# Kernel tuning notes

Measured on AMD Instinct MI355X. Metric: run time of the kernel, lower is better.

## Reference

```python
import jax, jax.numpy as jnp
import numpy as np

N, E, M, A, D = 100000, 3200000, 4096, 32, 16
G, V1, V2, O1 = 10, 20, 10, 20


def _lin(key, fin, fout, scale=0.1):
    kw, kb = jax.random.split(key)
    W = jax.random.normal(kw, (fin, fout), jnp.float32) * scale
    b = jax.random.normal(kb, (fout,), jnp.float32) * scale
    return W, b


def setup_inputs():
    key = jax.random.key(0)
    ks = jax.random.split(key, 32)
    inp = {}
    inp["x1"] = jax.random.normal(ks[0], (N, 15), jnp.float32)
    inp["x2"] = jax.random.normal(ks[1], (4,), jnp.float32)
    inp["edges"] = jax.random.randint(ks[2], (2, E), 0, N)
    inp["attack_src"] = jax.random.randint(ks[3], (M, A), 0, N)
    inp["attack_dst"] = jax.random.randint(ks[4], (M, A), 0, N)
    inp["attack_armies"] = jax.random.uniform(ks[5], (M, A), jnp.float32, 1.0, 20.0)
    inp["deploy_target"] = jax.random.randint(ks[6], (M, D), 0, N)
    inp["deploy_armies"] = jax.random.uniform(ks[7], (M, D), jnp.float32, 1.0, 10.0)
    inp["init_W"], inp["init_b"] = _lin(ks[8], 15, G)
    for i, fin in zip((1, 2, 3), (G + 15, 2 * G + 15, 3 * G + 15)):
        k1, k2, k3, k4 = jax.random.split(ks[8 + i], 4)
        inp[f"g{i}_Wl"] = jax.random.normal(k1, (fin, G), jnp.float32) * 0.1
        inp[f"g{i}_Wr"] = jax.random.normal(k2, (fin, G), jnp.float32) * 0.1
        inp[f"g{i}_att"] = jax.random.normal(k3, (G,), jnp.float32) * 0.1
        inp[f"g{i}_b"] = jax.random.normal(k4, (G,), jnp.float32) * 0.1
    inp["vt_W"], inp["vt_b"] = _lin(ks[12], 15 + G + 4, V1)
    inp["va_W"], inp["va_b"] = _lin(ks[13], V1, 1)
    inp["vv_W"], inp["vv_b"] = _lin(ks[14], V1, V2)
    inp["vl_W"], inp["vl_b"] = _lin(ks[15], V2, 1)
    inp["at_W"], inp["at_b"] = _lin(ks[16], 48, O1)
    inp["dt_W"], inp["dt_b"] = _lin(ks[17], 23, O1)
    inp["oa_W"], inp["oa_b"] = _lin(ks[18], O1, 1)
    inp["ov_W"], inp["ov_b"] = _lin(ks[19], O1, 1)
    return inp


def _gatv2(x, src, dst, Wl, Wr, att, bias, n):
    # GATv2 (PyG defaults: heads=1, negative_slope=0.2); dropout omitted (eval mode)
    xl = x @ Wl  # source-side transform  [N, G]
    xr = x @ Wr  # target-side transform  [N, G]
    e = jax.nn.leaky_relu(xl[src] + xr[dst], 0.2) @ att  # [Etot]
    emax = jax.ops.segment_max(e, dst, num_segments=n)
    ex = jnp.exp(e - emax[dst])
    denom = jax.ops.segment_sum(ex, dst, num_segments=n)
    alpha = ex / denom[dst]  # edge softmax per target node
    return jax.ops.segment_sum(alpha[:, None] * xl[src], dst, num_segments=n) + bias


def _forward(x1, x2, edges, attack_src, attack_dst, attack_armies,
             deploy_target, deploy_armies, p):
    n = x1.shape[0]
    loop = jnp.arange(n)
    src = jnp.concatenate([edges[0], loop])  # add_self_loops (PyG default)
    dst = jnp.concatenate([edges[1], loop])
    x_ = jax.nn.relu(x1 @ p["init_W"] + p["init_b"])  # Dropout = identity in eval
    xa = jax.nn.relu(_gatv2(jnp.concatenate([x_, x1], 1), src, dst,
                            p["g1_Wl"], p["g1_Wr"], p["g1_att"], p["g1_b"], n))
    xb = jax.nn.relu(_gatv2(jnp.concatenate([xa, x_, x1], 1), src, dst,
                            p["g2_Wl"], p["g2_Wr"], p["g2_att"], p["g2_b"], n))
    xc = jax.nn.relu(_gatv2(jnp.concatenate([xb, xa, x_, x1], 1), src, dst,
                            p["g3_Wl"], p["g3_Wr"], p["g3_att"], p["g3_b"], n))
    # per-move order features, batched over all moves at once: [M,A,*] / [M,D,*]
    x1d = x1[attack_dst]  # [M, A, 15]
    extra = 0.6 * attack_armies - 0.7 * (x1d[..., 3] + x1d[..., 4])
    att_feat = jnp.concatenate([xc[attack_src], xc[attack_dst],
                                x1[attack_src][..., 3:], x1d[..., 1:],
                                attack_armies[..., None], extra[..., None]], -1)  # [M,A,48]
    dep_feat = jnp.concatenate([xc[deploy_target], x1[deploy_target][..., 3:],
                                deploy_armies[..., None]], -1)  # [M,D,23]
    orders = jax.nn.relu(jnp.concatenate(
        [att_feat @ p["at_W"] + p["at_b"], dep_feat @ p["dt_W"] + p["dt_b"]], 1))  # [M,A+D,O1]
    oattn = jax.nn.softmax(orders @ p["oa_W"] + p["oa_b"], axis=1)  # softmax over orders
    pm = jnp.sum(oattn * (orders @ p["ov_W"] + p["ov_b"]), axis=(1, 2))  # [M]
    # value head: attention-pool over nodes
    vfeat = jnp.concatenate([xc, x1, jnp.tile(x2, (n, 1))], 1)  # [N, 29]
    v = jax.nn.relu(vfeat @ p["vt_W"] + p["vt_b"])
    vattn = jax.nn.softmax(v @ p["va_W"] + p["va_b"], axis=0)
    vagg = jax.nn.relu(jnp.sum(vattn * (v @ p["vv_W"] + p["vv_b"]), axis=0))
    V = jnp.tanh(vagg @ p["vl_W"] + p["vl_b"]).reshape(())
    return V, jax.nn.log_softmax(pm)


def reference(x1, x2, edges, attack_src, attack_dst, attack_armies,
              deploy_target, deploy_armies,
              init_W, init_b,
              g1_Wl, g1_Wr, g1_att, g1_b,
              g2_Wl, g2_Wr, g2_att, g2_b,
              g3_Wl, g3_Wr, g3_att, g3_b,
              vt_W, vt_b, va_W, va_b, vv_W, vv_b, vl_W, vl_b,
              at_W, at_b, dt_W, dt_b, oa_W, oa_b, ov_W, ov_b):
    p = dict(init_W=init_W, init_b=init_b,
             g1_Wl=g1_Wl, g1_Wr=g1_Wr, g1_att=g1_att, g1_b=g1_b,
             g2_Wl=g2_Wl, g2_Wr=g2_Wr, g2_att=g2_att, g2_b=g2_b,
             g3_Wl=g3_Wl, g3_Wr=g3_Wr, g3_att=g3_att, g3_b=g3_b,
             vt_W=vt_W, vt_b=vt_b, va_W=va_W, va_b=va_b, vv_W=vv_W, vv_b=vv_b,
             vl_W=vl_W, vl_b=vl_b, at_W=at_W, at_b=at_b, dt_W=dt_W, dt_b=dt_b,
             oa_W=oa_W, oa_b=oa_b, ov_W=ov_W, ov_b=ov_b)
    return _forward(x1, x2, edges, attack_src, attack_dst, attack_armies,
                    deploy_target, deploy_armies, p)
```

## Files before the change

kernel.cpp:

```cpp
#include <hip/hip_runtime.h>
#include <math.h>


#define PAD 12
#define LP 8
#define MAXB 784
#define CHK 8192

__device__ __forceinline__ float lrelu02(float v) { return v > 0.f ? v : 0.2f * v; }

__device__ __forceinline__ unsigned pk_bf16(float a, float b)
{
    unsigned ua = __float_as_uint(a), ub = __float_as_uint(b);
    ua += 0x7fffu + ((ua >> 16) & 1u);
    ub += 0x7fffu + ((ub >> 16) & 1u);
    return (ua >> 16) | (ub & 0xffff0000u);
}
__device__ __forceinline__ float bf_lo(unsigned u) { return __uint_as_float(u << 16); }
__device__ __forceinline__ float bf_hi(unsigned u) { return __uint_as_float(u & 0xffff0000u); }

template <int NS>
__device__ __forceinline__ void transform_body(
    int n, const float* __restrict__ s0, const float* __restrict__ s1,
    const float* __restrict__ s2, const float* __restrict__ x1,
    const float* __restrict__ Wl, const float* __restrict__ Wr,
    unsigned* __restrict__ XLb, float* __restrict__ XR)
{
    float al[10], ar[10];
#pragma unroll
    for (int g = 0; g < 10; ++g) { al[g] = 0.f; ar[g] = 0.f; }
    int o = 0;
#define TB_BLOCK(SP)                                                        \
    {                                                                       \
        const float4* pr = (const float4*)((SP) + n * PAD);                 \
        float4 v0 = pr[0], v1 = pr[1], v2 = pr[2];                          \
        float fv[10] = {v0.x, v0.y, v0.z, v0.w, v1.x, v1.y, v1.z, v1.w,     \
                        v2.x, v2.y};                                        \
        _Pragma("unroll") for (int k = 0; k < 10; ++k)                      \
        {                                                                   \
            _Pragma("unroll") for (int g = 0; g < 10; ++g)                  \
            {                                                               \
                al[g] += fv[k] * Wl[(o + k) * 10 + g];                      \
                ar[g] += fv[k] * Wr[(o + k) * 10 + g];                      \
            }                                                               \
        }                                                                   \
        o += 10;                                                            \
    }
    if constexpr (NS >= 1) TB_BLOCK(s0)
    if constexpr (NS >= 2) TB_BLOCK(s1)
    if constexpr (NS >= 3) TB_BLOCK(s2)
#undef TB_BLOCK
#pragma unroll
    for (int k = 0; k < 15; ++k) {
        float fv = x1[n * 15 + k];
#pragma unroll
        for (int g = 0; g < 10; ++g) {
            al[g] += fv * Wl[(o + k) * 10 + g];
            ar[g] += fv * Wr[(o + k) * 10 + g];
        }
    }
    uint4 q0;
    q0.x = pk_bf16(al[0], al[1]);
    q0.y = pk_bf16(al[2], al[3]);
    q0.z = pk_bf16(al[4], al[5]);
    q0.w = pk_bf16(al[6], al[7]);
    uint4 q1;
    q1.x = pk_bf16(al[8], al[9]);
    q1.y = 0; q1.z = 0; q1.w = 0;
    uint4* pb = (uint4*)(XLb + (size_t)n * LP);
    pb[0] = q0;
    pb[1] = q1;
    float4* po = (float4*)(XR + n * PAD);
    po[0] = make_float4(ar[0], ar[1], ar[2], ar[3]);
    po[1] = make_float4(ar[4], ar[5], ar[6], ar[7]);
    po[2] = make_float4(ar[8], ar[9], 0.f, 0.f);
}

__global__ __launch_bounds__(256) void k_a1_init(
    const int* __restrict__ edst, int E, unsigned short* __restrict__ pos,
    int* __restrict__ cntg, int PA,
    const float* __restrict__ x1, const float* __restrict__ W,
    const float* __restrict__ b, float* __restrict__ xo, int N, int NBK)
{
    if ((int)blockIdx.x < PA) {
        __shared__ int h[MAXB];
        for (int j = threadIdx.x; j < NBK; j += 256) h[j] = 0;
        __syncthreads();
        int base = blockIdx.x * CHK;
        for (int k = 0; k < CHK / 256; ++k) {
            int i = base + k * 256 + threadIdx.x;
            if (i < E) {
                int bkt = edst[i] >> 7;
                int p = atomicAdd(&h[bkt], 1);
                pos[i] = (unsigned short)p;
            }
        }
        __syncthreads();
        for (int j = threadIdx.x; j < NBK; j += 256)
            cntg[(size_t)j * PA + blockIdx.x] = h[j];
    } else {
        int n = ((int)blockIdx.x - PA) * 256 + (int)threadIdx.x;
        if (n >= N) return;
        float acc[10];
#pragma unroll
        for (int g = 0; g < 10; ++g) acc[g] = b[g];
#pragma unroll
        for (int k = 0; k < 15; ++k) {
            float fv = x1[n * 15 + k];
#pragma unroll
            for (int g = 0; g < 10; ++g) acc[g] += fv * W[k * 10 + g];
        }
        float4* po = (float4*)(xo + n * PAD);
        po[0] = make_float4(fmaxf(acc[0], 0.f), fmaxf(acc[1], 0.f),
                            fmaxf(acc[2], 0.f), fmaxf(acc[3], 0.f));
        po[1] = make_float4(fmaxf(acc[4], 0.f), fmaxf(acc[5], 0.f),
                            fmaxf(acc[6], 0.f), fmaxf(acc[7], 0.f));
        po[2] = make_float4(fmaxf(acc[8], 0.f), fmaxf(acc[9], 0.f), 0.f, 0.f);
    }
}

__global__ __launch_bounds__(1024) void k_scanA(
    const int* __restrict__ cntg, int* __restrict__ bases,
    int* __restrict__ bsumA, int TOT)
{
    __shared__ int wsum[16];
    int t = threadIdx.x;
    int i = blockIdx.x * 1024 + t;
    int lane = t & 63, w = t >> 6;
    int x = (i < TOT) ? cntg[i] : 0;
    int incl = x;
#pragma unroll
    for (int off = 1; off < 64; off <<= 1) {
        int u = __shfl_up(incl, off);
        if (lane >= off) incl += u;
    }
    if (lane == 63) wsum[w] = incl;
    __syncthreads();
    int woff = 0;
    for (int k = 0; k < w; ++k) woff += wsum[k];
    incl += woff;
    if (i < TOT) bases[i] = incl - x;
    if (t == 1023) bsumA[blockIdx.x] = incl;
}

__global__ __launch_bounds__(512) void k_scanB(
    const int* __restrict__ bsumA, int* __restrict__ boffA, int NBLKA,
    float* __restrict__ vsums, int* __restrict__ rowptr, int N, int Etot)
{
    __shared__ int wsum[8];
    int t = threadIdx.x;
    int lane = t & 63, w = t >> 6;
    int x = (t < NBLKA) ? bsumA[t] : 0;
    int incl = x;
#pragma unroll
    for (int off = 1; off < 64; off <<= 1) {
        int u = __shfl_up(incl, off);
        if (lane >= off) incl += u;
    }
    if (lane == 63) wsum[w] = incl;
    __syncthreads();
    int woff = 0;
    for (int k = 0; k < w; ++k) woff += wsum[k];
    incl += woff;
    if (t < NBLKA) boffA[t] = incl - x;
    if (t < 16) vsums[t] = 0.f;
    if (t == 0) rowptr[N] = Etot;
}

__global__ __launch_bounds__(1024) void k_scanC(
    int* __restrict__ bases, const int* __restrict__ boffA, int TOT)
{
    int i = blockIdx.x * 1024 + threadIdx.x;
    if (i < TOT) bases[i] += boffA[blockIdx.x];
}

__global__ __launch_bounds__(256) void k_a2(
    const int* __restrict__ esrc, const int* __restrict__ edst, int E,
    const int* __restrict__ bases, const unsigned short* __restrict__ pos,
    unsigned* __restrict__ pairs, int PA)
{
    int i = blockIdx.x * 256 + threadIdx.x;
    if (i >= E) return;
    int d = edst[i], s = esrc[i];
    int bkt = d >> 7;
    int blk = i / CHK;
    int dest = bases[(size_t)bkt * PA + blk] + (int)pos[i];
    pairs[dest] = (unsigned)s | ((unsigned)(d & 127) << 17);
}

__global__ __launch_bounds__(256) void k_b_tr1(
    const unsigned* __restrict__ pairs, const int* __restrict__ bases,
    int* __restrict__ rowptr, int* __restrict__ deg, int* __restrict__ sidx,
    int N, int NBK, int PA, int E,
    const float* __restrict__ s0a, const float* __restrict__ x1,
    const float* __restrict__ Wl, const float* __restrict__ Wr,
    unsigned* __restrict__ XLb, float* __restrict__ XR, int NB)
{
    if ((int)blockIdx.x < NBK) {
        __shared__ int cnt[128];
        __shared__ int cur[128];
        __shared__ int wtot;
        int t = threadIdx.x;
        if (t < 128) cnt[t] = 0;
        __syncthreads();
        int b = blockIdx.x;
        int p0 = bases[(size_t)b * PA];
        int p1 = (b + 1 < NBK) ? bases[(size_t)(b + 1) * PA] : E;
        int n0 = b << 7;
        int nn = N - n0; nn = nn < 0 ? 0 : (nn > 128 ? 128 : nn);
        for (int i = p0 + t; i < p1; i += 256) atomicAdd(&cnt[pairs[i] >> 17], 1);
        __syncthreads();
        int x = 0, incl = 0;
        if (t < 128) {
            x = cnt[t] + (t < nn ? 1 : 0);
            incl = x;
            int lane = t & 63;
#pragma unroll
            for (int off = 1; off < 64; off <<= 1) {
                int u = __shfl_up(incl, off);
                if (lane >= off) incl += u;
            }
            if (t == 63) wtot = incl;
        }
        __syncthreads();
        int sb = p0 + (b << 7);
        if (t < 128) {
            if (t >= 64) incl += wtot;
            int st = incl - x;
            if (t < nn) {
                int r = sb + st;
                rowptr[n0 + t] = r;
                deg[n0 + t] = cnt[t] + 1;
                sidx[r] = n0 + t;
                cur[t] = st + 1;
            } else {
                cur[t] = st;
            }
        }
        __syncthreads();
        for (int i = p0 + t; i < p1; i += 256) {
            unsigned w = pairs[i];
            int l = w >> 17, s = w & 0x1FFFF;
            int off = atomicAdd(&cur[l], 1);
            sidx[sb + off] = s;
        }
    } else {
        int n = ((int)blockIdx.x - NBK) * 256 + (int)threadIdx.x;
        if (n >= N) return;
        transform_body<1>(n, s0a, nullptr, nullptr, x1, Wl, Wr, XLb, XR);
    }
}

template <int NS>
__global__ __launch_bounds__(256) void k_transform(
    const float* __restrict__ s0, const float* __restrict__ s1,
    const float* __restrict__ s2, const float* __restrict__ x1,
    const float* __restrict__ Wl, const float* __restrict__ Wr,
    unsigned* __restrict__ XLb, float* __restrict__ XR, int N)
{
    int n = blockIdx.x * blockDim.x + threadIdx.x;
    if (n >= N) return;
    transform_body<NS>(n, s0, s1, s2, x1, Wl, Wr, XLb, XR);
}

__global__ __launch_bounds__(256) void k_gather(
    const int* __restrict__ rowptr, const int* __restrict__ deg,
    const int* __restrict__ sidx,
    const unsigned* __restrict__ XLb, const float* __restrict__ XR,
    const float* __restrict__ att, const float* __restrict__ b,
    float* __restrict__ xo, int N)
{
    int node = blockIdx.x * 16 + (threadIdx.x >> 4);
    int l16 = threadIdx.x & 15;
    float acc[10];
#pragma unroll
    for (int g = 0; g < 10; ++g) acc[g] = 0.f;
    float den = 0.f;
    float satt[10];
#pragma unroll
    for (int g = 0; g < 10; ++g) satt[g] = att[g];
    if (node < N) {
        const float4* pr = (const float4*)(XR + node * PAD);
        float4 r0 = pr[0], r1 = pr[1], r2 = pr[2];
        float xr[10] = {r0.x, r0.y, r0.z, r0.w, r1.x, r1.y, r1.z, r1.w, r2.x, r2.y};
        int start = rowptr[node];
        int dgr = deg[node];
        int j = l16;
        while (j + 16 < dgr) {
            int s0 = sidx[start + j];
            int s1 = sidx[start + j + 16];
            const unsigned* pl0 = XLb + (size_t)s0 * LP;
            const unsigned* pl1 = XLb + (size_t)s1 * LP;
            uint4 qa = *(const uint4*)pl0;
            unsigned qa4 = pl0[4];
            uint4 qb = *(const uint4*)pl1;
            unsigned qb4 = pl1[4];
            float xa[10] = {bf_lo(qa.x), bf_hi(qa.x), bf_lo(qa.y), bf_hi(qa.y),
                            bf_lo(qa.z), bf_hi(qa.z), bf_lo(qa.w), bf_hi(qa.w),
                            bf_lo(qa4), bf_hi(qa4)};
            float xb[10] = {bf_lo(qb.x), bf_hi(qb.x), bf_lo(qb.y), bf_hi(qb.y),
                            bf_lo(qb.z), bf_hi(qb.z), bf_lo(qb.w), bf_hi(qb.w),
                            bf_lo(qb4), bf_hi(qb4)};
            float ea = 0.f, eb = 0.f;
#pragma unroll
            for (int g = 0; g < 10; ++g) {
                ea += lrelu02(xa[g] + xr[g]) * satt[g];
                eb += lrelu02(xb[g] + xr[g]) * satt[g];
            }
            float exa = __expf(ea), exb = __expf(eb);
#pragma unroll
            for (int g = 0; g < 10; ++g) acc[g] += exa * xa[g] + exb * xb[g];
            den += exa + exb;
            j += 32;
        }
        if (j < dgr) {
            int s = sidx[start + j];
            const unsigned* pl = XLb + (size_t)s * LP;
            uint4 q = *(const uint4*)pl;
            unsigned q4 = pl[4];
            float xl[10] = {bf_lo(q.x), bf_hi(q.x), bf_lo(q.y), bf_hi(q.y),
                            bf_lo(q.z), bf_hi(q.z), bf_lo(q.w), bf_hi(q.w),
                            bf_lo(q4), bf_hi(q4)};
            float e = 0.f;
#pragma unroll
            for (int g = 0; g < 10; ++g) e += lrelu02(xl[g] + xr[g]) * satt[g];
            float ex = __expf(e);
#pragma unroll
            for (int g = 0; g < 10; ++g) acc[g] += ex * xl[g];
            den += ex;
        }
    }
#pragma unroll
    for (int off = 1; off < 16; off <<= 1) {
        den += __shfl_xor(den, off);
#pragma unroll
        for (int g = 0; g < 10; ++g) acc[g] += __shfl_xor(acc[g], off);
    }
    if (node < N && l16 == 0) {
        float inv = 1.f / den;
        float r[10];
#pragma unroll
        for (int g = 0; g < 10; ++g) r[g] = fmaxf(acc[g] * inv + b[g], 0.f);
        float4* po = (float4*)(xo + node * PAD);
        po[0] = make_float4(r[0], r[1], r[2], r[3]);
        po[1] = make_float4(r[4], r[5], r[6], r[7]);
        po[2] = make_float4(r[8], r[9], 0.f, 0.f);
    }
}

__global__ __launch_bounds__(256) void k_scores(
    const float* __restrict__ xc, const float* __restrict__ x1,
    const float* __restrict__ x2,
    const int* __restrict__ asrc, const int* __restrict__ adst,
    const float* __restrict__ aarm,
    const int* __restrict__ dtgt, const float* __restrict__ darm,
    const float* __restrict__ atW, const float* __restrict__ atb,
    const float* __restrict__ dtW, const float* __restrict__ dtb,
    const float* __restrict__ oaW, const float* __restrict__ oab,
    const float* __restrict__ ovW, const float* __restrict__ ovb,
    const float* __restrict__ vtW, const float* __restrict__ vtb,
    const float* __restrict__ vaW, const float* __restrict__ vab,
    const float* __restrict__ vvW, const float* __restrict__ vvb,
    float* __restrict__ vsums, float2* __restrict__ OS,
    int AB, int DB, int NB, int N, int M)
{
    if ((int)blockIdx.x < AB) {
        int i = blockIdx.x * 256 + threadIdx.x;
        if (i >= M * 32) return;
        int m = i >> 5, a = i & 31;
        int s = asrc[i], d = adst[i];
        float arm = aarm[i];
        float ord[20];
#pragma unroll
        for (int j = 0; j < 20; ++j) ord[j] = atb[j];
        {
            const float4* pc = (const float4*)(xc + s * PAD);
            float4 c0 = pc[0], c1 = pc[1], c2 = pc[2];
            float fv[10] = {c0.x, c0.y, c0.z, c0.w, c1.x, c1.y, c1.z, c1.w,
                            c2.x, c2.y};
#pragma unroll
            for (int k = 0; k < 10; ++k)
#pragma unroll
                for (int j = 0; j < 20; ++j) ord[j] += fv[k] * atW[k * 20 + j];
        }
        {
            const float4* pc = (const float4*)(xc + d * PAD);
            float4 c0 = pc[0], c1 = pc[1], c2 = pc[2];
            float fv[10] = {c0.x, c0.y, c0.z, c0.w, c1.x, c1.y, c1.z, c1.w,
                            c2.x, c2.y};
#pragma unroll
            for (int k = 0; k < 10; ++k)
#pragma unroll
                for (int j = 0; j < 20; ++j)
                    ord[j] += fv[k] * atW[(10 + k) * 20 + j];
        }
#pragma unroll
        for (int k = 0; k < 12; ++k) {
            float fv = x1[s * 15 + 3 + k];
#pragma unroll
            for (int j = 0; j < 20; ++j) ord[j] += fv * atW[(20 + k) * 20 + j];
        }
        float d3 = 0.f, d4 = 0.f;
#pragma unroll
        for (int k = 0; k < 14; ++k) {
            float fv = x1[d * 15 + 1 + k];
            if (k == 2) d3 = fv;
            if (k == 3) d4 = fv;
#pragma unroll
            for (int j = 0; j < 20; ++j) ord[j] += fv * atW[(32 + k) * 20 + j];
        }
        float extra = 0.6f * arm - 0.7f * (d3 + d4);
#pragma unroll
        for (int j = 0; j < 20; ++j)
            ord[j] += arm * atW[46 * 20 + j] + extra * atW[47 * 20 + j];
        float asc = oab[0], vsc = ovb[0];
#pragma unroll
        for (int j = 0; j < 20; ++j) {
            float oj = fmaxf(ord[j], 0.f);
            asc += oj * oaW[j];
            vsc += oj * ovW[j];
        }
        OS[(size_t)m * 48 + a] = make_float2(asc, vsc);
    } else if ((int)blockIdx.x < AB + DB) {
        int i = ((int)blockIdx.x - AB) * 256 + threadIdx.x;
        if (i >= M * 16) return;
        int m = i >> 4, dd = i & 15;
        int tg = dtgt[i];
        float arm = darm[i];
        float ord[20];
#pragma unroll
        for (int j = 0; j < 20; ++j) ord[j] = dtb[j];
        {
            const float4* pc = (const float4*)(xc + tg * PAD);
            float4 c0 = pc[0], c1 = pc[1], c2 = pc[2];
            float fv[10] = {c0.x, c0.y, c0.z, c0.w, c1.x, c1.y, c1.z, c1.w,
                            c2.x, c2.y};
#pragma unroll
            for (int k = 0; k < 10; ++k)
#pragma unroll
                for (int j = 0; j < 20; ++j) ord[j] += fv[k] * dtW[k * 20 + j];
        }
#pragma unroll
        for (int k = 0; k < 12; ++k) {
            float fv = x1[tg * 15 + 3 + k];
#pragma unroll
            for (int j = 0; j < 20; ++j) ord[j] += fv * dtW[(10 + k) * 20 + j];
        }
#pragma unroll
        for (int j = 0; j < 20; ++j) ord[j] += arm * dtW[22 * 20 + j];
        float asc = oab[0], vsc = ovb[0];
#pragma unroll
        for (int j = 0; j < 20; ++j) {
            float oj = fmaxf(ord[j], 0.f);
            asc += oj * oaW[j];
            vsc += oj * ovW[j];
        }
        OS[(size_t)m * 48 + 32 + dd] = make_float2(asc, vsc);
    } else {
        __shared__ float sred[4][11];
        int t = threadIdx.x;
        int n = ((int)blockIdx.x - AB - DB) * 256 + t;
        float w = 0.f;
        float wv[10];
#pragma unroll
        for (int c = 0; c < 10; ++c) wv[c] = 0.f;
        if (n < N) {
            float v[20];
#pragma unroll
            for (int j = 0; j < 20; ++j) v[j] = vtb[j];
            {
                const float4* pc = (const float4*)(xc + n * PAD);
                float4 c0 = pc[0], c1 = pc[1], c2 = pc[2];
                float fv[10] = {c0.x, c0.y, c0.z, c0.w, c1.x, c1.y, c1.z, c1.w,
                                c2.x, c2.y};
#pragma unroll
                for (int k = 0; k < 10; ++k)
#pragma unroll
                    for (int j = 0; j < 20; ++j) v[j] += fv[k] * vtW[k * 20 + j];
            }
#pragma unroll
            for (int k = 0; k < 15; ++k) {
                float fv = x1[n * 15 + k];
#pragma unroll
                for (int j = 0; j < 20; ++j) v[j] += fv * vtW[(10 + k) * 20 + j];
            }
#pragma unroll
            for (int k = 0; k < 4; ++k) {
                float fv = x2[k];
#pragma unroll
                for (int j = 0; j < 20; ++j) v[j] += fv * vtW[(25 + k) * 20 + j];
            }
            float sc = vab[0];
#pragma unroll
            for (int j = 0; j < 20; ++j) {
                v[j] = fmaxf(v[j], 0.f);
                sc += v[j] * vaW[j];
            }
            w = __expf(sc);
#pragma unroll
            for (int c = 0; c < 10; ++c) {
                float t2 = vvb[c];
#pragma unroll
                for (int j = 0; j < 20; ++j) t2 += v[j] * vvW[j * 10 + c];
                wv[c] = w * t2;
            }
        }
#pragma unroll
        for (int off = 32; off > 0; off >>= 1) {
            w += __shfl_xor(w, off);
#pragma unroll
            for (int c = 0; c < 10; ++c) wv[c] += __shfl_xor(wv[c], off);
        }
        int wave = t >> 6, lane = t & 63;
        if (lane == 0) {
            sred[wave][0] = w;
#pragma unroll
            for (int c = 0; c < 10; ++c) sred[wave][1 + c] = wv[c];
        }
        __syncthreads();
        if (t == 0) {
#pragma unroll
            for (int c = 0; c < 11; ++c) {
                float s = sred[0][c] + sred[1][c] + sred[2][c] + sred[3][c];
                atomicAdd(&vsums[c], s);
            }
        }
    }
}

__global__ __launch_bounds__(256) void k_moves(
    const float2* __restrict__ OS, float* __restrict__ pm, int M)
{
    int m = blockIdx.x * 256 + threadIdx.x;
    if (m >= M) return;
    const float2* p = OS + (size_t)m * 48;
    float mx = -1e30f;
#pragma unroll
    for (int o = 0; o < 48; ++o) mx = fmaxf(mx, p[o].x);
    float Z = 0.f, num = 0.f;
#pragma unroll
    for (int o = 0; o < 48; ++o) {
        float e = __expf(p[o].x - mx);
        Z += e;
        num += e * p[o].y;
    }
    pm[m] = num / Z;
}

__global__ __launch_bounds__(1024) void k_final(
    const float* __restrict__ pm, const float* __restrict__ vsums,
    const float* __restrict__ vlW, const float* __restrict__ vlb,
    float* __restrict__ out, int M)
{
    __shared__ float red[16];
    __shared__ float sval;
    int t = threadIdx.x;
    int wave = t >> 6, lane = t & 63;
    if (t == 1023) {
        float inv = 1.f / vsums[0];
        float V = vlb[0];
#pragma unroll
        for (int j = 0; j < 10; ++j) V += fmaxf(vsums[1 + j] * inv, 0.f) * vlW[j];
        out[0] = tanhf(V);
    }
    float mx = -1e30f;
    for (int i = t; i < M; i += 1024) mx = fmaxf(mx, pm[i]);
#pragma unroll
    for (int off = 32; off > 0; off >>= 1) mx = fmaxf(mx, __shfl_xor(mx, off));
    if (lane == 0) red[wave] = mx;
    __syncthreads();
    if (t == 0) {
        float m2 = red[0];
        for (int i = 1; i < 16; ++i) m2 = fmaxf(m2, red[i]);
        sval = m2;
    }
    __syncthreads();
    float smax = sval;
    float sum = 0.f;
    for (int i = t; i < M; i += 1024) sum += __expf(pm[i] - smax);
#pragma unroll
    for (int off = 32; off > 0; off >>= 1) sum += __shfl_xor(sum, off);
    if (lane == 0) red[wave] = sum;
    __syncthreads();
    if (t == 0) {
        float s2 = 0.f;
        for (int i = 0; i < 16; ++i) s2 += red[i];
        sval = s2;
    }
    __syncthreads();
    float lse = smax + logf(sval);
    for (int i = t; i < M; i += 1024) out[1 + i] = pm[i] - lse;
}

extern "C" void kernel_launch(void* const* d_in, const int* in_sizes, int n_in,
                              void* d_out, int out_size, void* d_ws, size_t ws_size,
                              hipStream_t stream)
{
    const float* x1   = (const float*)d_in[0];
    const float* x2   = (const float*)d_in[1];
    const int*   edges = (const int*)d_in[2];
    const int*   asrc = (const int*)d_in[3];
    const int*   adst = (const int*)d_in[4];
    const float* aarm = (const float*)d_in[5];
    const int*   dtgt = (const int*)d_in[6];
    const float* darm = (const float*)d_in[7];
    const float* initW = (const float*)d_in[8];
    const float* initb = (const float*)d_in[9];
    const float* g1Wl = (const float*)d_in[10];
    const float* g1Wr = (const float*)d_in[11];
    const float* g1att = (const float*)d_in[12];
    const float* g1b = (const float*)d_in[13];
    const float* g2Wl = (const float*)d_in[14];
    const float* g2Wr = (const float*)d_in[15];
    const float* g2att = (const float*)d_in[16];
    const float* g2b = (const float*)d_in[17];
    const float* g3Wl = (const float*)d_in[18];
    const float* g3Wr = (const float*)d_in[19];
    const float* g3att = (const float*)d_in[20];
    const float* g3b = (const float*)d_in[21];
    const float* vtW = (const float*)d_in[22];
    const float* vtb = (const float*)d_in[23];
    const float* vaW = (const float*)d_in[24];
    const float* vab = (const float*)d_in[25];
    const float* vvW = (const float*)d_in[26];
    const float* vvb = (const float*)d_in[27];
    const float* vlW = (const float*)d_in[28];
    const float* vlb = (const float*)d_in[29];
    const float* atW = (const float*)d_in[30];
    const float* atb = (const float*)d_in[31];
    const float* dtW = (const float*)d_in[32];
    const float* dtb = (const float*)d_in[33];
    const float* oaW = (const float*)d_in[34];
    const float* oab = (const float*)d_in[35];
    const float* ovW = (const float*)d_in[36];
    const float* ovb = (const float*)d_in[37];

    const int N = in_sizes[0] / 15;
    const int E = in_sizes[2] / 2;
    const int M = in_sizes[3] / 32;
    const int Etot = E + N;
    const int NBK = (N + 127) >> 7;
    const int PA = (E + CHK - 1) / CHK;
    const int TOT = NBK * PA;

    float* ws = (float*)d_ws;
    size_t off = 0;
    float* XU = ws + off; off += (size_t)N * PAD;
    float* XA = ws + off; off += (size_t)N * PAD;
    float* XB = ws + off; off += (size_t)N * PAD;
    float* XC = ws + off; off += (size_t)N * PAD;
    unsigned* XLb = (unsigned*)(ws + off); off += (size_t)N * LP;
    float* XR = ws + off; off += (size_t)N * PAD;
    int* sidx = (int*)(ws + off); off += Etot;
    unsigned* pairs = (unsigned*)(ws + off); off += E;
    int* deg = (int*)(ws + off); off += N;
    int* rowptr = (int*)(ws + off); off += N + 8;
    int* cntg = (int*)(ws + off); off += TOT + 8;
    int* bases = (int*)(ws + off); off += TOT + 8;
    int* bsumA = (int*)(ws + off); off += 512;
    int* boffA = (int*)(ws + off); off += 512;
    float* VS = ws + off; off += 16;
    float* PM = ws + off; off += M;
    float2* OS = (float2*)(ws + off); off += (size_t)M * 48 * 2;
    unsigned short* pos = (unsigned short*)XA;

    float* outp = (float*)d_out;

    const int NB = (N + 255) / 256;
    const int NG = (N + 15) / 16;
    const int AB = (M * 32 + 255) / 256;
    const int DB = (M * 16 + 255) / 256;
    const int SCA = (TOT + 1023) / 1024;
    const int* esrc = edges;
    const int* edst = edges + E;

    k_a1_init<<<PA + NB, 256, 0, stream>>>(edst, E, pos, cntg, PA,
                                           x1, initW, initb, XU, N, NBK);
    k_scanA<<<SCA, 1024, 0, stream>>>(cntg, bases, bsumA, TOT);
    k_scanB<<<1, 512, 0, stream>>>(bsumA, boffA, SCA, VS, rowptr, N, Etot);
    k_scanC<<<SCA, 1024, 0, stream>>>(bases, boffA, TOT);
    k_a2<<<(E + 255) / 256, 256, 0, stream>>>(esrc, edst, E, bases, pos, pairs, PA);
    k_b_tr1<<<NBK + NB, 256, 0, stream>>>(pairs, bases, rowptr, deg, sidx, N, NBK, PA, E,
                                          XU, x1, g1Wl, g1Wr, XLb, XR, NB);
    k_gather<<<NG, 256, 0, stream>>>(rowptr, deg, sidx, XLb, XR, g1att, g1b, XA, N);

    k_transform<2><<<NB, 256, 0, stream>>>(XA, XU, nullptr, x1, g2Wl, g2Wr, XLb, XR, N);
    k_gather<<<NG, 256, 0, stream>>>(rowptr, deg, sidx, XLb, XR, g2att, g2b, XB, N);

    k_transform<3><<<NB, 256, 0, stream>>>(XB, XA, XU, x1, g3Wl, g3Wr, XLb, XR, N);
    k_gather<<<NG, 256, 0, stream>>>(rowptr, deg, sidx, XLb, XR, g3att, g3b, XC, N);

    k_scores<<<AB + DB + NB, 256, 0, stream>>>(XC, x1, x2, asrc, adst, aarm,
                                               dtgt, darm, atW, atb, dtW, dtb,
                                               oaW, oab, ovW, ovb,
                                               vtW, vtb, vaW, vab, vvW, vvb,
                                               VS, OS, AB, DB, NB, N, M);
    k_moves<<<(M + 255) / 256, 256, 0, stream>>>(OS, PM, M);
    k_final<<<1, 1024, 0, stream>>>(PM, VS, vlW, vlb, outp, M);
}
```

Before: 405.2 us.

## Locally sort edge chunks in shared memory before scattering to bucket pairs

The scatter pass now re-histograms each edge chunk in LDS, scans the bucket counts locally, and sorts the chunk's edges by bucket in shared memory before writing them. Writes to the global pairs array therefore land in contiguous runs per bucket instead of random addresses, and the global pos array is no longer needed. The chunk size is halved so the larger per-block shared memory fits and there are more blocks, which doubles the number of partial histograms to scan. The first layer transform moves to run alongside this scatter pass instead of the CSR build, adding LDS use and an extra block-wide scan per chunk.

```diff
diff --git a/kernel.cpp b/kernel.cpp
--- a/kernel.cpp
+++ b/kernel.cpp
@@ -5,7 +5,7 @@
 #define PAD 12
 #define LP 8
 #define MAXB 784
-#define CHK 8192
+#define CHK 4096
 
 __device__ __forceinline__ float lrelu02(float v) { return v > 0.f ? v : 0.2f * v; }
 
@@ -77,8 +77,7 @@
 }
 
 __global__ __launch_bounds__(256) void k_a1_init(
-    const int* __restrict__ edst, int E, unsigned short* __restrict__ pos,
-    int* __restrict__ cntg, int PA,
+    const int* __restrict__ edst, int E, int* __restrict__ cntg, int PA,
     const float* __restrict__ x1, const float* __restrict__ W,
     const float* __restrict__ b, float* __restrict__ xo, int N, int NBK)
 {
@@ -89,11 +88,7 @@
         int base = blockIdx.x * CHK;
         for (int k = 0; k < CHK / 256; ++k) {
             int i = base + k * 256 + threadIdx.x;
-            if (i < E) {
-                int bkt = edst[i] >> 7;
-                int p = atomicAdd(&h[bkt], 1);
-                pos[i] = (unsigned short)p;
-            }
+            if (i < E) atomicAdd(&h[edst[i] >> 7], 1);
         }
         __syncthreads();
         for (int j = threadIdx.x; j < NBK; j += 256)
@@ -143,11 +138,11 @@
     if (t == 1023) bsumA[blockIdx.x] = incl;
 }
 
-__global__ __launch_bounds__(512) void k_scanB(
+__global__ __launch_bounds__(1024) void k_scanB(
     const int* __restrict__ bsumA, int* __restrict__ boffA, int NBLKA,
     float* __restrict__ vsums, int* __restrict__ rowptr, int N, int Etot)
 {
-    __shared__ int wsum[8];
+    __shared__ int wsum[16];
     int t = threadIdx.x;
     int lane = t & 63, w = t >> 6;
     int x = (t < NBLKA) ? bsumA[t] : 0;
@@ -174,80 +169,140 @@
     if (i < TOT) bases[i] += boffA[blockIdx.x];
 }
 
-__global__ __launch_bounds__(256) void k_a2(
+__global__ __launch_bounds__(256) void k_a2tr1(
     const int* __restrict__ esrc, const int* __restrict__ edst, int E,
-    const int* __restrict__ bases, const unsigned short* __restrict__ pos,
-    unsigned* __restrict__ pairs, int PA)
-{
-    int i = blockIdx.x * 256 + threadIdx.x;
-    if (i >= E) return;
-    int d = edst[i], s = esrc[i];
-    int bkt = d >> 7;
-    int blk = i / CHK;
-    int dest = bases[(size_t)bkt * PA + blk] + (int)pos[i];
-    pairs[dest] = (unsigned)s | ((unsigned)(d & 127) << 17);
-}
-
-__global__ __launch_bounds__(256) void k_b_tr1(
-    const unsigned* __restrict__ pairs, const int* __restrict__ bases,
-    int* __restrict__ rowptr, int* __restrict__ deg, int* __restrict__ sidx,
-    int N, int NBK, int PA, int E,
+    const int* __restrict__ bases, unsigned* __restrict__ pairs, int PA,
     const float* __restrict__ s0a, const float* __restrict__ x1,
     const float* __restrict__ Wl, const float* __restrict__ Wr,
-    unsigned* __restrict__ XLb, float* __restrict__ XR, int NB)
-{
-    if ((int)blockIdx.x < NBK) {
-        __shared__ int cnt[128];
-        __shared__ int cur[128];
-        __shared__ int wtot;
+    unsigned* __restrict__ XLb, float* __restrict__ XR, int N, int NBK)
+{
+    __shared__ int h[MAXB];
+    __shared__ unsigned tmp[CHK];
+    __shared__ unsigned vals[CHK];
+    __shared__ unsigned short bkt16[CHK];
+    __shared__ int wtotS[4];
+    if ((int)blockIdx.x < PA) {
         int t = threadIdx.x;
-        if (t < 128) cnt[t] = 0;
+        for (int j = t; j < NBK; j += 256) h[j] = 0;
         __syncthreads();
-        int b = blockIdx.x;
-        int p0 = bases[(size_t)b * PA];
-        int p1 = (b + 1 < NBK) ? bases[(size_t)(b + 1) * PA] : E;
-        int n0 = b << 7;
-        int nn = N - n0; nn = nn < 0 ? 0 : (nn > 128 ? 128 : nn);
-        for (int i = p0 + t; i < p1; i += 256) atomicAdd(&cnt[pairs[i] >> 17], 1);
+        int base = blockIdx.x * CHK;
+        int nE = E - base; nE = nE > CHK ? CHK : nE;
+        for (int k = 0; k < CHK / 256; ++k) {
+            int e = k * 256 + t;
+            if (e < nE) {
+                unsigned dv = (unsigned)edst[base + e];
+                int p = atomicAdd(&h[dv >> 7], 1);
+                tmp[e] = dv | ((unsigned)p << 17);
+            }
+        }
         __syncthreads();
-        int x = 0, incl = 0;
-        if (t < 128) {
-            x = cnt[t] + (t < nn ? 1 : 0);
-            incl = x;
-            int lane = t & 63;
+        {
+            int j = t * 4;
+            int v0 = 0, v1 = 0, v2 = 0, v3 = 0;
+            if (j < NBK) v0 = h[j];
+            if (j + 1 < NBK) v1 = h[j + 1];
+            if (j + 2 < NBK) v2 = h[j + 2];
+            if (j + 3 < NBK) v3 = h[j + 3];
+            int s = v0 + v1 + v2 + v3;
+            int lane = t & 63, wv = t >> 6;
+            int incl = s;
 #pragma unroll
             for (int off = 1; off < 64; off <<= 1) {
                 int u = __shfl_up(incl, off);
                 if (lane >= off) incl += u;
             }
-            if (t == 63) wtot = incl;
+            if (lane == 63) wtotS[wv] = incl;
+            __syncthreads();
+            int woff = 0;
+            for (int k2 = 0; k2 < wv; ++k2) woff += wtotS[k2];
+            int ebase = incl - s + woff;
+            __syncthreads();
+            if (j < NBK) h[j] = ebase;
+            if (j + 1 < NBK) h[j + 1] = ebase + v0;
+            if (j + 2 < NBK) h[j + 2] = ebase + v0 + v1;
+            if (j + 3 < NBK) h[j + 3] = ebase + v0 + v1 + v2;
         }
         __syncthreads();
-        int sb = p0 + (b << 7);
-        if (t < 128) {
-            if (t >= 64) incl += wtot;
-            int st = incl - x;
-            if (t < nn) {
-                int r = sb + st;
-                rowptr[n0 + t] = r;
-                deg[n0 + t] = cnt[t] + 1;
-                sidx[r] = n0 + t;
-                cur[t] = st + 1;
-            } else {
-                cur[t] = st;
+        for (int k = 0; k < CHK / 256; ++k) {
+            int e = k * 256 + t;
+            if (e < nE) {
+                unsigned w = tmp[e];
+                unsigned dv = w & 0x1FFFFu;
+                int p = (int)(w >> 17);
+                int b = (int)(dv >> 7);
+                int slot = h[b] + p;
+                vals[slot] = (unsigned)esrc[base + e] | ((dv & 127u) << 17);
+                bkt16[slot] = (unsigned short)b;
             }
         }
         __syncthreads();
-        for (int i = p0 + t; i < p1; i += 256) {
-            unsigned w = pairs[i];
-            int l = w >> 17, s = w & 0x1FFFF;
-            int off = atomicAdd(&cur[l], 1);
-            sidx[sb + off] = s;
+        for (int k = 0; k < CHK / 256; ++k) {
+            int e = k * 256 + t;
+            if (e < nE) {
+                int b = (int)bkt16[e];
+                int within = e - h[b];
+                int dest = bases[(size_t)b * PA + blockIdx.x] + within;
+                pairs[dest] = vals[e];
+            }
         }
     } else {
-        int n = ((int)blockIdx.x - NBK) * 256 + (int)threadIdx.x;
+        int n = ((int)blockIdx.x - PA) * 256 + (int)threadIdx.x;
         if (n >= N) return;
         transform_body<1>(n, s0a, nullptr, nullptr, x1, Wl, Wr, XLb, XR);
+    }
+}
+
+__global__ __launch_bounds__(256) void k_b(
+    const unsigned* __restrict__ pairs, const int* __restrict__ bases,
+    int* __restrict__ rowptr, int* __restrict__ deg, int* __restrict__ sidx,
+    int N, int NBK, int PA, int E)
+{
+    __shared__ int cnt[128];
+    __shared__ int cur[128];
+    __shared__ int wtot;
+    int t = threadIdx.x;
+    if (t < 128) cnt[t] = 0;
+    __syncthreads();
+    int b = blockIdx.x;
+    int p0 = bases[(size_t)b * PA];
+    int p1 = (b + 1 < NBK) ? bases[(size_t)(b + 1) * PA] : E;
+    int n0 = b << 7;
+    int nn = N - n0; nn = nn < 0 ? 0 : (nn > 128 ? 128 : nn);
+    for (int i = p0 + t; i < p1; i += 256) atomicAdd(&cnt[pairs[i] >> 17], 1);
+    __syncthreads();
+    int x = 0, incl = 0;
+    if (t < 128) {
+        x = cnt[t] + (t < nn ? 1 : 0);
+        incl = x;
+        int lane = t & 63;
+#pragma unroll
+        for (int off = 1; off < 64; off <<= 1) {
+            int u = __shfl_up(incl, off);
+            if (lane >= off) incl += u;
+        }
+        if (t == 63) wtot = incl;
+    }
+    __syncthreads();
+    int sb = p0 + (b << 7);
+    if (t < 128) {
+        if (t >= 64) incl += wtot;
+        int st = incl - x;
+        if (t < nn) {
+            int r = sb + st;
+            rowptr[n0 + t] = r;
+            deg[n0 + t] = cnt[t] + 1;
+            sidx[r] = n0 + t;
+            cur[t] = st + 1;
+        } else {
+            cur[t] = st;
+        }
+    }
+    __syncthreads();
+    for (int i = p0 + t; i < p1; i += 256) {
+        unsigned w = pairs[i];
+        int l = w >> 17, s = w & 0x1FFFF;
+        int off = atomicAdd(&cur[l], 1);
+        sidx[sb + off] = s;
     }
 }
 
@@ -657,12 +712,11 @@
     int* rowptr = (int*)(ws + off); off += N + 8;
     int* cntg = (int*)(ws + off); off += TOT + 8;
     int* bases = (int*)(ws + off); off += TOT + 8;
-    int* bsumA = (int*)(ws + off); off += 512;
-    int* boffA = (int*)(ws + off); off += 512;
+    int* bsumA = (int*)(ws + off); off += 1024;
+    int* boffA = (int*)(ws + off); off += 1024;
     float* VS = ws + off; off += 16;
     float* PM = ws + off; off += M;
     float2* OS = (float2*)(ws + off); off += (size_t)M * 48 * 2;
-    unsigned short* pos = (unsigned short*)XA;
 
     float* outp = (float*)d_out;
 
@@ -674,14 +728,14 @@
     const int* esrc = edges;
     const int* edst = edges + E;
 
-    k_a1_init<<<PA + NB, 256, 0, stream>>>(edst, E, pos, cntg, PA,
+    k_a1_init<<<PA + NB, 256, 0, stream>>>(edst, E, cntg, PA,
                                            x1, initW, initb, XU, N, NBK);
     k_scanA<<<SCA, 1024, 0, stream>>>(cntg, bases, bsumA, TOT);
-    k_scanB<<<1, 512, 0, stream>>>(bsumA, boffA, SCA, VS, rowptr, N, Etot);
+    k_scanB<<<1, 1024, 0, stream>>>(bsumA, boffA, SCA, VS, rowptr, N, Etot);
     k_scanC<<<SCA, 1024, 0, stream>>>(bases, boffA, TOT);
-    k_a2<<<(E + 255) / 256, 256, 0, stream>>>(esrc, edst, E, bases, pos, pairs, PA);
-    k_b_tr1<<<NBK + NB, 256, 0, stream>>>(pairs, bases, rowptr, deg, sidx, N, NBK, PA, E,
-                                          XU, x1, g1Wl, g1Wr, XLb, XR, NB);
+    k_a2tr1<<<PA + NB, 256, 0, stream>>>(esrc, edst, E, bases, pairs, PA,
+                                         XU, x1, g1Wl, g1Wr, XLb, XR, N, NBK);
+    k_b<<<NBK, 256, 0, stream>>>(pairs, bases, rowptr, deg, sidx, N, NBK, PA, E);
     k_gather<<<NG, 256, 0, stream>>>(rowptr, deg, sidx, XLb, XR, g1att, g1b, XA, N);
 
     k_transform<2><<<NB, 256, 0, stream>>>(XA, XU, nullptr, x1, g2Wl, g2Wr, XLb, XR, N);
```

New measurement: 422.4 us. 1.04x slower.
